# Kernel tuning notes

Measured on AMD Instinct MI355X. Metric: run time of the kernel, lower is better.

Reference implementation:

```python
import jax, jax.numpy as jnp
import numpy as np

B, L, HID = 2, 2048, 4096
NH, NKV, HD = 16, 4, 64
BLOCK = 16
THETA = 8000000.0
EPS = 1e-6
NEG = jnp.finfo(jnp.float32).min


def _rope_tables(theta, L, hd):
    inv_freq = 1.0 / (theta ** (np.arange(0, hd, 2, dtype=np.float32) / hd))  # [hd/2]
    t = np.arange(L, dtype=np.float32)
    freqs = np.outer(t, inv_freq)                      # [L, hd/2]
    emb = np.concatenate([freqs, freqs], axis=-1)      # [L, hd]
    return jnp.asarray(np.cos(emb)), jnp.asarray(np.sin(emb))


def setup_inputs() -> dict:
    key = jax.random.key(0)
    k1, k2, k3 = jax.random.split(key, 3)
    hidden_states = jax.random.normal(k1, (B, L, HID), dtype=jnp.float32)
    Wqkv = jax.random.normal(k2, (HID, (NH + 2 * NKV) * HD), dtype=jnp.float32) * 0.006
    Wo = jax.random.normal(k3, (NH * HD, HID), dtype=jnp.float32) * 0.006
    q_norm_w = jnp.ones((HD,), dtype=jnp.float32)
    k_norm_w = jnp.ones((HD,), dtype=jnp.float32)
    # block-diagonal causal additive mask [1,1,L,L]
    idx = jnp.arange(L)
    same_block = (idx[:, None] // BLOCK) == (idx[None, :] // BLOCK)
    causal = idx[:, None] >= idx[None, :]
    attention_mask = jnp.where(same_block & causal, 0.0, NEG)[None, None].astype(jnp.float32)
    cos1, sin1 = _rope_tables(THETA, L, HD)
    cos = jnp.broadcast_to(cos1[None], (B, L, HD))
    sin = jnp.broadcast_to(sin1[None], (B, L, HD))
    return {"hidden_states": hidden_states, "attention_mask": attention_mask,
            "cos": cos, "sin": sin, "Wqkv": Wqkv, "Wo": Wo,
            "q_norm_w": q_norm_w, "k_norm_w": k_norm_w}


def _rms_norm(x, w):
    xf = x.astype(jnp.float32)
    var = jnp.mean(xf * xf, axis=-1, keepdims=True)
    return (xf * jax.lax.rsqrt(var + EPS)).astype(x.dtype) * w


def _rotate_half(x):
    x1, x2 = jnp.split(x, 2, axis=-1)
    return jnp.concatenate([-x2, x1], axis=-1)


def reference(hidden_states, attention_mask, cos, sin, Wqkv, Wo, q_norm_w, k_norm_w):
    Bc, Lc, _ = hidden_states.shape
    qkv = hidden_states @ Wqkv                                # [B,L,(NH+2NKV)*HD]
    qkv = qkv.reshape(Bc, Lc, NH + 2 * NKV, HD)
    q, k, v = jnp.split(qkv, [NH, NH + NKV], axis=2)
    q = q.transpose(0, 2, 1, 3)                               # [B,NH,L,HD]
    k = k.transpose(0, 2, 1, 3)                               # [B,NKV,L,HD]
    v = v.transpose(0, 2, 1, 3)
    q = _rms_norm(q, q_norm_w)
    k = _rms_norm(k, k_norm_w)
    c = cos[:, None]                                          # [B,1,L,HD]
    s = sin[:, None]
    q = q * c + _rotate_half(q) * s
    k = k * c + _rotate_half(k) * s
    groups = NH // NKV
    k = jnp.repeat(k, groups, axis=1)                         # [B,NH,L,HD]
    v = jnp.repeat(v, groups, axis=1)
    scale = 1.0 / jnp.sqrt(jnp.float32(HD))
    scores = jnp.einsum('bhqd,bhkd->bhqk', q, k) * scale + attention_mask
    probs = jax.nn.softmax(scores, axis=-1)
    out = jnp.einsum('bhqk,bhkd->bhqd', probs, v)             # [B,NH,L,HD]
    out = out.transpose(0, 2, 1, 3).reshape(Bc, Lc, NH * HD)
    return out @ Wo
```

## Files before the change

### kernel.cpp

```cpp
#include <hip/hip_runtime.h>
#include <hip/hip_bf16.h>
#include <cstdint>

#define B_SZ   2
#define L_SEQ  2048
#define HID    4096
#define NH     16
#define NKV    4
#define HD     64
#define NQKV   (NH + 2*NKV)
#define QKV_N  (NQKV*HD)
#define O_N    (NH*HD)
#define M_ROWS (B_SZ*L_SEQ)
#define EPSV   1e-6f

typedef __bf16  bf16x8_t  __attribute__((ext_vector_type(8)));
typedef float   f32x4_t   __attribute__((ext_vector_type(4)));
typedef unsigned short ushort8_t __attribute__((ext_vector_type(8)));

__device__ __forceinline__ unsigned short f2b(float f) {
    union { float f; uint32_t u; } v; v.f = f;
    uint32_t r = v.u + 0x7FFFu + ((v.u >> 16) & 1u);
    return (unsigned short)(r >> 16);
}
__device__ __forceinline__ float b2f(unsigned short u) {
    union { uint32_t u; float f; } v; v.u = ((uint32_t)u) << 16;
    return v.f;
}

__device__ __forceinline__ void gload_lds16(const void* g, void* l) {
    __builtin_amdgcn_global_load_lds(
        (__attribute__((address_space(1))) void*)(g),
        (__attribute__((address_space(3))) void*)(l),
        16, 0, 0);
}

#define BARF() do { asm volatile("" ::: "memory"); \
                    __builtin_amdgcn_s_barrier();  \
                    asm volatile("" ::: "memory"); } while (0)

template <int N> __device__ __forceinline__ void vmcnt_wait() {
    if constexpr (N == 4)       asm volatile("s_waitcnt vmcnt(4)"  ::: "memory");
    else if constexpr (N == 5)  asm volatile("s_waitcnt vmcnt(5)"  ::: "memory");
    else if constexpr (N == 6)  asm volatile("s_waitcnt vmcnt(6)"  ::: "memory");
    else if constexpr (N == 8)  asm volatile("s_waitcnt vmcnt(8)"  ::: "memory");
    else if constexpr (N == 12) asm volatile("s_waitcnt vmcnt(12)" ::: "memory");
    else                        asm volatile("s_waitcnt vmcnt(0)"  ::: "memory");
}

__global__ __launch_bounds__(256) void cvt_f32_bf16(const float* __restrict__ in,
                                                    unsigned short* __restrict__ out,
                                                    int n8) {
    int i = blockIdx.x * 256 + threadIdx.x;
    if (i >= n8) return;
    const float4* p = (const float4*)(in + (size_t)i * 8);
    float4 a = p[0], b = p[1];
    ushort8_t o;
    o[0]=f2b(a.x); o[1]=f2b(a.y); o[2]=f2b(a.z); o[3]=f2b(a.w);
    o[4]=f2b(b.x); o[5]=f2b(b.y); o[6]=f2b(b.z); o[7]=f2b(b.w);
    *(ushort8_t*)(out + (size_t)i * 8) = o;
}

__global__ __launch_bounds__(256) void transpose_both(const float* __restrict__ Wqkv,
                                                      unsigned short* __restrict__ WqkvT,
                                                      const float* __restrict__ Wo,
                                                      unsigned short* __restrict__ WoT) {
    __shared__ float t[32][33];
    const float* in;
    unsigned short* out;
    int R, C, bx, by;
    if (blockIdx.x < 6144) {
        in = Wqkv; out = WqkvT; R = HID; C = QKV_N;
        bx = blockIdx.x % 48; by = blockIdx.x / 48;
    } else {
        int b = blockIdx.x - 6144;
        in = Wo; out = WoT; R = O_N; C = HID;
        bx = b % 128; by = b / 128;
    }
    const int c0 = bx * 32;
    const int r0 = by * 32;
    const int tx = threadIdx.x & 31;
    const int ty = threadIdx.x >> 5;
    #pragma unroll
    for (int i = 0; i < 32; i += 8)
        t[ty + i][tx] = in[(size_t)(r0 + ty + i) * C + c0 + tx];
    __syncthreads();
    #pragma unroll
    for (int i = 0; i < 32; i += 8)
        out[(size_t)(c0 + ty + i) * R + r0 + tx] = f2b(t[tx][ty + i]);
}

template <int BM, int BN, int BK, int NBUF, int NWM, int NWN, bool OBF16, typename OutT>
__global__ __launch_bounds__(512, 2)
void gemm_sb(const unsigned short* __restrict__ A,
             const unsigned short* __restrict__ Bt,
             OutT* __restrict__ C, int M, int N, int K) {
    constexpr int WM    = BM / NWM;
    constexpr int WN    = BN / NWN;
    constexpr int AF    = WM / 16;
    constexpr int BF    = WN / 16;
    constexpr int KK    = BK / 32;
    constexpr int BUF   = (BM + BN) * BK;
    constexpr int ROWS  = 4096 / BK;
    constexpr int AR    = BM / ROWS;
    constexpr int BR    = BN / ROWS;
    constexpr int RNDS  = AR + BR;
    constexpr int DEPTH = NBUF - 2;

    __shared__ unsigned short smem[NBUF * BUF];

    const int tid  = threadIdx.x;
    const int lane = tid & 63;
    const int wave = tid >> 6;
    const int wm   = wave / NWN;
    const int wn   = wave % NWN;
    const int fr   = lane & 15;
    const int fq   = lane >> 4;

    const int nbx = N / BN;
    int bid = blockIdx.x;
    const int cpx = gridDim.x >> 3;
    bid = (bid & 7) * cpx + (bid >> 3);
    const int bx = bid % nbx, by = bid / nbx;
    const int m0 = by * BM, n0 = bx * BN;

    const int srow = tid / (BK / 8);
    const int sch  = tid & (BK / 8 - 1);
    const int ssw  = (BK == 64) ? (srow & 7) : ((srow >> 1) & 3);
    const int scs  = (sch ^ ssw) << 3;
    const unsigned short* gA = A  + (size_t)(m0 + srow) * K + scs;
    const unsigned short* gB = Bt + (size_t)(n0 + srow) * K + scs;

    const int frsw = (BK == 64) ? (fr & 7) : ((fr >> 1) & 3);

    f32x4_t acc[AF][BF];
    #pragma unroll
    for (int m = 0; m < AF; m++)
        #pragma unroll
        for (int n = 0; n < BF; n++)
            acc[m][n] = (f32x4_t){0.f, 0.f, 0.f, 0.f};

    const int NT = K / BK;

    auto STAGE = [&](int T) {
        const int pb = (T % NBUF) * BUF;
        #pragma unroll
        for (int q = 0; q < AR; ++q)
            gload_lds16(gA + (size_t)(q * ROWS) * K + (size_t)T * BK,
                        &smem[pb + q * 4096 + tid * 8]);
        #pragma unroll
        for (int q = 0; q < BR; ++q)
            gload_lds16(gB + (size_t)(q * ROWS) * K + (size_t)T * BK,
                        &smem[pb + BM * BK + q * 4096 + tid * 8]);
    };

    #pragma unroll
    for (int pt = 0; pt < NBUF - 1; ++pt) STAGE(pt);
    vmcnt_wait<DEPTH * RNDS>();

    for (int t = 0; t < NT; ++t) {
        const int sb = (t % NBUF) * BUF;
        BARF();

        #pragma unroll
        for (int kk = 0; kk < KK; ++kk) {
            const int cxk = (((kk * 4 + fq) ^ frsw)) << 3;
            bf16x8_t aF[AF], bF[BF];
            #pragma unroll
            for (int mm = 0; mm < AF; ++mm)
                aF[mm] = *(const bf16x8_t*)&smem[sb + (wm*WM + mm*16 + fr)*BK + cxk];
            #pragma unroll
            for (int nn = 0; nn < BF; ++nn)
                bF[nn] = *(const bf16x8_t*)&smem[sb + BM*BK + (wn*WN + nn*16 + fr)*BK + cxk];

            if (kk == 0 && t + NBUF - 1 < NT) STAGE(t + NBUF - 1);

            __builtin_amdgcn_s_setprio(1);
            #pragma unroll
            for (int mm = 0; mm < AF; ++mm)
                #pragma unroll
                for (int nn = 0; nn < BF; ++nn)
                    acc[mm][nn] = __builtin_amdgcn_mfma_f32_16x16x32_bf16(
                        aF[mm], bF[nn], acc[mm][nn], 0, 0, 0);
            __builtin_amdgcn_s_setprio(0);
        }

        if constexpr (DEPTH == 2) {
            if (t + 3 < NT)      { vmcnt_wait<2 * RNDS>(); }
            else if (t + 2 < NT) { vmcnt_wait<RNDS>(); }
            else if (t + 1 < NT) { vmcnt_wait<0>(); }
        } else {
            if (t + 2 < NT)      { vmcnt_wait<RNDS>(); }
            else if (t + 1 < NT) { vmcnt_wait<0>(); }
        }
    }

    const int crow = m0 + wm * WM + fq * 4;
    const int ccol = n0 + wn * WN + fr;
    #pragma unroll
    for (int m = 0; m < AF; m++)
        #pragma unroll
        for (int n = 0; n < BF; n++)
            #pragma unroll
            for (int rr = 0; rr < 4; rr++) {
                const size_t idx = (size_t)(crow + m*16 + rr) * N + ccol + n*16;
                if constexpr (OBF16) C[idx] = (OutT)f2b(acc[m][n][rr]);
                else                 C[idx] = (OutT)acc[m][n][rr];
            }
}

__global__ __launch_bounds__(64) void attn_fused(const unsigned short* __restrict__ qkv,
                                                 const float* __restrict__ cosb,
                                                 const float* __restrict__ sinb,
                                                 const float* __restrict__ qw,
                                                 const float* __restrict__ kw,
                                                 unsigned short* __restrict__ out) {
    const int h    = blockIdx.x & (NH - 1);
    const int blk  = (blockIdx.x >> 4) & 127;
    const int b    = blockIdx.x >> 11;
    const int pos0 = blk * 16;
    const int kvh  = h >> 2;

    const int lane = threadIdx.x;
    const int r    = lane >> 2;
    const int qp   = lane & 3;
    const int d0   = qp * 16;

    __shared__ float qs[16][65];
    __shared__ float ks[16][65];
    __shared__ float vs[16][65];
    __shared__ float ps[16][17];

    const size_t rowb = ((size_t)(b * L_SEQ + pos0 + r)) * NQKV;
    const unsigned short* qptr = qkv + (rowb + h) * HD + d0;
    const unsigned short* kptr = qkv + (rowb + NH + kvh) * HD + d0;
    const unsigned short* vptr = qkv + (rowb + NH + NKV + kvh) * HD + d0;
    const size_t csrow = ((size_t)(b * L_SEQ + pos0 + r)) * HD + d0;

    float q[16], k[16], v[16], cs[16], sn[16];
    {
        ushort8_t q0 = *(const ushort8_t*)&qptr[0], q1 = *(const ushort8_t*)&qptr[8];
        ushort8_t k0 = *(const ushort8_t*)&kptr[0], k1 = *(const ushort8_t*)&kptr[8];
        ushort8_t v0 = *(const ushort8_t*)&vptr[0], v1 = *(const ushort8_t*)&vptr[8];
        #pragma unroll
        for (int i = 0; i < 8; i++) {
            q[i] = b2f(q0[i]); q[i+8] = b2f(q1[i]);
            k[i] = b2f(k0[i]); k[i+8] = b2f(k1[i]);
            v[i] = b2f(v0[i]); v[i+8] = b2f(v1[i]);
        }
        #pragma unroll
        for (int i = 0; i < 16; i += 4) {
            *(float4*)&cs[i] = *(const float4*)&cosb[csrow + i];
            *(float4*)&sn[i] = *(const float4*)&sinb[csrow + i];
        }
    }

    float sq = 0.f, sk = 0.f;
    #pragma unroll
    for (int i = 0; i < 16; i++) { sq += q[i]*q[i]; sk += k[i]*k[i]; }
    sq += __shfl_xor(sq, 1); sq += __shfl_xor(sq, 2);
    sk += __shfl_xor(sk, 1); sk += __shfl_xor(sk, 2);
    const float rq = rsqrtf(sq * (1.f / HD) + EPSV);
    const float rk = rsqrtf(sk * (1.f / HD) + EPSV);

    const float sgn = (qp < 2) ? -1.f : 1.f;
    #pragma unroll
    for (int i = 0; i < 16; i++) {
        float qn = q[i] * rq * qw[d0 + i];
        float kn = k[i] * rk * kw[d0 + i];
        float qo = __shfl_xor(qn, 2);
        float ko = __shfl_xor(kn, 2);
        qs[r][d0 + i] = qn * cs[i] + sgn * qo * sn[i];
        ks[r][d0 + i] = kn * cs[i] + sgn * ko * sn[i];
        vs[r][d0 + i] = v[i];
    }
    __syncthreads();

    float sc[4] = {0.f, 0.f, 0.f, 0.f};
    for (int d = 0; d < 64; d++) {
        const float qd = qs[r][d];
        sc[0] += qd * ks[qp     ][d];
        sc[1] += qd * ks[qp +  4][d];
        sc[2] += qd * ks[qp +  8][d];
        sc[3] += qd * ks[qp + 12][d];
    }
    #pragma unroll
    for (int cc = 0; cc < 4; cc++) {
        const int c = qp + cc * 4;
        sc[cc] = (c <= r) ? sc[cc] * 0.125f : -3.0e38f;
    }
    float mx = fmaxf(fmaxf(sc[0], sc[1]), fmaxf(sc[2], sc[3]));
    mx = fmaxf(mx, __shfl_xor(mx, 1));
    mx = fmaxf(mx, __shfl_xor(mx, 2));
    float e[4], sum = 0.f;
    #pragma unroll
    for (int cc = 0; cc < 4; cc++) { e[cc] = __expf(sc[cc] - mx); sum += e[cc]; }
    sum += __shfl_xor(sum, 1); sum += __shfl_xor(sum, 2);
    const float inv = 1.f / sum;
    #pragma unroll
    for (int cc = 0; cc < 4; cc++) ps[r][qp + cc * 4] = e[cc] * inv;
    __syncthreads();

    float o[16];
    #pragma unroll
    for (int i = 0; i < 16; i++) o[i] = 0.f;
    #pragma unroll
    for (int c = 0; c < 16; c++) {
        const float p = ps[r][c];
        #pragma unroll
        for (int i = 0; i < 16; i++) o[i] += p * vs[c][d0 + i];
    }

    __attribute__((aligned(16))) unsigned short ob[16];
    #pragma unroll
    for (int i = 0; i < 16; i++) ob[i] = f2b(o[i]);
    unsigned short* optr = out + (((size_t)(b * L_SEQ + pos0 + r) * NH + h) * HD) + d0;
    *(uint4*)optr       = *(uint4*)&ob[0];
    *((uint4*)optr + 1) = *(uint4*)&ob[8];
}

extern "C" void kernel_launch(void* const* d_in, const int* in_sizes, int n_in,
                              void* d_out, int out_size, void* d_ws, size_t ws_size,
                              hipStream_t stream) {
    const float* hid  = (const float*)d_in[0];
    const float* cosb = (const float*)d_in[2];
    const float* sinb = (const float*)d_in[3];
    const float* Wqkv = (const float*)d_in[4];
    const float* Wo   = (const float*)d_in[5];
    const float* qw   = (const float*)d_in[6];
    const float* kw   = (const float*)d_in[7];
    float* outp = (float*)d_out;

    char* ws = (char*)d_ws;
    unsigned short* Hb    = (unsigned short*)ws; ws += (size_t)M_ROWS * HID * 2;
    unsigned short* WqkvT = (unsigned short*)ws; ws += (size_t)QKV_N * HID * 2;
    unsigned short* WoT   = (unsigned short*)ws; ws += (size_t)HID * O_N * 2;
    unsigned short* qkvb  = (unsigned short*)ws; ws += (size_t)M_ROWS * QKV_N * 2;
    unsigned short* attnb = (unsigned short*)ws;

    {
        int n8 = (M_ROWS * HID) / 8;
        cvt_f32_bf16<<<(n8 + 255) / 256, 256, 0, stream>>>(hid, Hb, n8);
    }
    transpose_both<<<dim3(6144 + 4096), 256, 0, stream>>>(Wqkv, WqkvT, Wo, WoT);

    gemm_sb<128, 192, 64, 3, 2, 4, true, unsigned short>
        <<<dim3((M_ROWS / 128) * (QKV_N / 192)), 512, 0, stream>>>
        (Hb, WqkvT, qkvb, M_ROWS, QKV_N, HID);

    attn_fused<<<dim3(B_SZ * (L_SEQ / 16) * NH), 64, 0, stream>>>(qkvb, cosb, sinb, qw, kw, attnb);

    gemm_sb<256, 256, 32, 4, 2, 4, false, float>
        <<<dim3((M_ROWS / 256) * (HID / 256)), 512, 0, stream>>>
        (attnb, WoT, outp, M_ROWS, HID, O_N);
}
```

Baseline: 145.8 us.

## Replace output-projection GEMM with 8-phase ping-pong pipelined kernel

Swaps the generic gemm_sb used for the Wo projection for a specialized 256x256 tile kernel with a BK=64 double-buffered LDS, XOR-swizzled layout, and an 8-phase schedule that interleaves direct global-to-LDS loads with MFMA groups, using s_setprio around the math. It also remaps block IDs across 8 groups for L2 locality. The goal is better overlap of memory and compute in the second GEMM, at the cost of many barriers and 64KB of LDS per block, which may limit occupancy.

```diff
diff --git a/kernel.cpp b/kernel.cpp
--- a/kernel.cpp
+++ b/kernel.cpp
@@ -38,6 +38,7 @@
 #define BARF() do { asm volatile("" ::: "memory"); \
                     __builtin_amdgcn_s_barrier();  \
                     asm volatile("" ::: "memory"); } while (0)
+#define LGKMW() asm volatile("s_waitcnt lgkmcnt(0)" ::: "memory")
 
 template <int N> __device__ __forceinline__ void vmcnt_wait() {
     if constexpr (N == 4)       asm volatile("s_waitcnt vmcnt(4)"  ::: "memory");
@@ -209,6 +210,120 @@
             }
 }
 
+#define G2_BUF 32768
+
+__global__ __launch_bounds__(512, 2)
+void gemm2_8p(const unsigned short* __restrict__ A,
+              const unsigned short* __restrict__ Bt,
+              float* __restrict__ C) {
+    constexpr int K     = O_N;
+    constexpr int N     = HID;
+    constexpr int NT    = K / 64;
+    constexpr int NITER = NT / 2;
+
+    __shared__ unsigned short smem[2 * G2_BUF];
+
+    const int tid  = threadIdx.x;
+    const int lane = tid & 63;
+    const int wave = tid >> 6;
+    const int wm   = wave >> 2;
+    const int wn   = wave & 3;
+    const int fr   = lane & 15;
+    const int fq   = lane >> 4;
+
+    const int nbx = N >> 8;
+    int bid = blockIdx.x;
+    const int cpx = gridDim.x >> 3;
+    bid = (bid & 7) * cpx + (bid >> 3);
+    const int bx = bid % nbx, by = bid / nbx;
+    const int m0 = by << 8, n0 = bx << 8;
+
+    const int srow = tid >> 3;
+    const int scs  = ((tid & 7) ^ (srow & 7)) << 3;
+    const unsigned short* gA = A  + (size_t)(m0 + srow) * K + scs;
+    const unsigned short* gB = Bt + (size_t)(n0 + srow) * K + scs;
+    const int frsw = fr & 7;
+
+    f32x4_t acc[8][4];
+    #pragma unroll
+    for (int m = 0; m < 8; m++)
+        #pragma unroll
+        for (int n = 0; n < 4; n++)
+            acc[m][n] = (f32x4_t){0.f, 0.f, 0.f, 0.f};
+
+#define SA(T, q) gload_lds16(gA + (size_t)((q)*64)*K + (size_t)(T)*64, \
+                             &smem[((T)&1)*G2_BUF + (q)*4096 + tid*8])
+#define SB(T, q) gload_lds16(gB + (size_t)((q)*64)*K + (size_t)(T)*64, \
+                             &smem[((T)&1)*G2_BUF + 16384 + (q)*4096 + tid*8])
+#define RDA(T, MH, KI) { _Pragma("unroll") for (int mm = 0; mm < 4; ++mm) { \
+    const int ro = ((T)&1)*G2_BUF + (wm*128 + (MH)*64 + mm*16 + fr)*64; \
+    aF[mm] = *(const bf16x8_t*)&smem[ro + ((((KI)*4 + fq) ^ frsw) << 3)]; } }
+#define RDB(T, KI, dst) { _Pragma("unroll") for (int nn = 0; nn < 4; ++nn) { \
+    const int ro = ((T)&1)*G2_BUF + 16384 + (wn*64 + nn*16 + fr)*64; \
+    dst[nn] = *(const bf16x8_t*)&smem[ro + ((((KI)*4 + fq) ^ frsw) << 3)]; } }
+#define MM16(MH, BS) { __builtin_amdgcn_s_setprio(1); \
+    _Pragma("unroll") for (int mm = 0; mm < 4; ++mm) \
+    _Pragma("unroll") for (int nn = 0; nn < 4; ++nn) \
+        acc[(MH)*4 + mm][nn] = __builtin_amdgcn_mfma_f32_16x16x32_bf16( \
+            aF[mm], BS[nn], acc[(MH)*4 + mm][nn], 0, 0, 0); \
+    __builtin_amdgcn_s_setprio(0); }
+
+    SA(0,0); SA(0,1); SA(0,2); SA(0,3);
+    SB(0,0); SB(0,1); SB(0,2); SB(0,3);
+    SA(1,0); SA(1,2); SB(1,0); SB(1,1);
+    vmcnt_wait<4>();
+    BARF();
+
+    for (int i = 0; i < NITER; ++i) {
+        const int t0 = 2*i, t1 = 2*i + 1;
+        bf16x8_t aF[4], b0[4], b1[4];
+
+        RDA(t0, 0, 0); RDB(t0, 0, b0);
+        SA(t1, 1); SA(t1, 3);
+        BARF(); LGKMW(); MM16(0, b0); BARF();
+        RDA(t0, 0, 1); RDB(t0, 1, b1);
+        SB(t1, 2); SB(t1, 3);
+        BARF(); LGKMW(); MM16(0, b1); BARF();
+        RDA(t0, 1, 0);
+        if (t0 + 2 < NT) { SA(t0 + 2, 0); SA(t0 + 2, 2); }
+        BARF(); LGKMW(); MM16(1, b0); BARF();
+        RDA(t0, 1, 1);
+        if (t0 + 2 < NT) { SB(t0 + 2, 0); SB(t0 + 2, 1); }
+        BARF(); LGKMW(); MM16(1, b1);
+        if (i + 1 < NITER) { vmcnt_wait<4>(); } else { vmcnt_wait<0>(); }
+        BARF();
+        RDA(t1, 0, 0); RDB(t1, 0, b0);
+        if (t0 + 2 < NT) { SA(t0 + 2, 1); SA(t0 + 2, 3); }
+        BARF(); LGKMW(); MM16(0, b0); BARF();
+        RDA(t1, 0, 1); RDB(t1, 1, b1);
+        if (t0 + 2 < NT) { SB(t0 + 2, 2); SB(t0 + 2, 3); }
+        BARF(); LGKMW(); MM16(0, b1); BARF();
+        RDA(t1, 1, 0);
+        if (t1 + 2 < NT) { SA(t1 + 2, 0); SA(t1 + 2, 2); }
+        BARF(); LGKMW(); MM16(1, b0); BARF();
+        RDA(t1, 1, 1);
+        if (t1 + 2 < NT) { SB(t1 + 2, 0); SB(t1 + 2, 1); }
+        BARF(); LGKMW(); MM16(1, b1);
+        if (i + 1 < NITER) { vmcnt_wait<4>(); }
+        BARF();
+    }
+#undef SA
+#undef SB
+#undef RDA
+#undef RDB
+#undef MM16
+
+    const int crow = m0 + wm * 128 + fq * 4;
+    const int ccol = n0 + wn * 64 + fr;
+    #pragma unroll
+    for (int m = 0; m < 8; m++)
+        #pragma unroll
+        for (int n = 0; n < 4; n++)
+            #pragma unroll
+            for (int rr = 0; rr < 4; rr++)
+                C[(size_t)(crow + m*16 + rr) * N + ccol + n*16] = acc[m][n][rr];
+}
+
 __global__ __launch_bounds__(64) void attn_fused(const unsigned short* __restrict__ qkv,
                                                  const float* __restrict__ cosb,
                                                  const float* __restrict__ sinb,
@@ -350,7 +465,6 @@
 
     attn_fused<<<dim3(B_SZ * (L_SEQ / 16) * NH), 64, 0, stream>>>(qkvb, cosb, sinb, qw, kw, attnb);
 
-    gemm_sb<256, 256, 32, 4, 2, 4, false, float>
-        <<<dim3((M_ROWS / 256) * (HID / 256)), 512, 0, stream>>>
-        (attnb, WoT, outp, M_ROWS, HID, O_N);
-}
+    gemm2_8p<<<dim3((M_ROWS / 256) * (HID / 256)), 512, 0, stream>>>
+        (attnb, WoT, outp);
+}
```

New measurement: 144.5 us. About the same (-0.9%).

## Add dedicated 128x128 output-projection GEMM and merge prep kernels into one launch

Applied to the files above, without the earlier changes.

Replaces the generic 256x256-tile output projection GEMM with a specialized 128x128-tile kernel. It uses 256 threads, double-buffered direct-to-LDS loads, an XOR-swizzled LDS layout and an LDS-staged coalesced float4 epilogue, giving four times more blocks for better CU occupancy and load balance. It also fuses the hidden-state conversion and weight transpose into a single prep launch to cut launch overhead. The smaller tile lowers data reuse per block, and the two-stage pipeline with full vmcnt waits may expose memory latency.

```diff
diff --git a/kernel.cpp b/kernel.cpp
--- a/kernel.cpp
+++ b/kernel.cpp
@@ -38,6 +38,7 @@
 #define BARF() do { asm volatile("" ::: "memory"); \
                     __builtin_amdgcn_s_barrier();  \
                     asm volatile("" ::: "memory"); } while (0)
+#define LGKMW() asm volatile("s_waitcnt lgkmcnt(0)" ::: "memory")
 
 template <int N> __device__ __forceinline__ void vmcnt_wait() {
     if constexpr (N == 4)       asm volatile("s_waitcnt vmcnt(4)"  ::: "memory");
@@ -48,34 +49,35 @@
     else                        asm volatile("s_waitcnt vmcnt(0)"  ::: "memory");
 }
 
-__global__ __launch_bounds__(256) void cvt_f32_bf16(const float* __restrict__ in,
-                                                    unsigned short* __restrict__ out,
-                                                    int n8) {
-    int i = blockIdx.x * 256 + threadIdx.x;
-    if (i >= n8) return;
-    const float4* p = (const float4*)(in + (size_t)i * 8);
-    float4 a = p[0], b = p[1];
-    ushort8_t o;
-    o[0]=f2b(a.x); o[1]=f2b(a.y); o[2]=f2b(a.z); o[3]=f2b(a.w);
-    o[4]=f2b(b.x); o[5]=f2b(b.y); o[6]=f2b(b.z); o[7]=f2b(b.w);
-    *(ushort8_t*)(out + (size_t)i * 8) = o;
-}
-
-__global__ __launch_bounds__(256) void transpose_both(const float* __restrict__ Wqkv,
-                                                      unsigned short* __restrict__ WqkvT,
-                                                      const float* __restrict__ Wo,
-                                                      unsigned short* __restrict__ WoT) {
+#define CVT_BLKS 8192
+__global__ __launch_bounds__(256) void prep(const float* __restrict__ hid,
+                                            unsigned short* __restrict__ Hb,
+                                            const float* __restrict__ Wqkv,
+                                            unsigned short* __restrict__ WqkvT,
+                                            const float* __restrict__ Wo,
+                                            unsigned short* __restrict__ WoT) {
+    if (blockIdx.x < CVT_BLKS) {
+        int i = blockIdx.x * 256 + threadIdx.x;
+        const float4* p = (const float4*)(hid + (size_t)i * 8);
+        float4 a = p[0], b = p[1];
+        ushort8_t o;
+        o[0]=f2b(a.x); o[1]=f2b(a.y); o[2]=f2b(a.z); o[3]=f2b(a.w);
+        o[4]=f2b(b.x); o[5]=f2b(b.y); o[6]=f2b(b.z); o[7]=f2b(b.w);
+        *(ushort8_t*)(Hb + (size_t)i * 8) = o;
+        return;
+    }
     __shared__ float t[32][33];
     const float* in;
     unsigned short* out;
     int R, C, bx, by;
-    if (blockIdx.x < 6144) {
+    int blk = blockIdx.x - CVT_BLKS;
+    if (blk < 6144) {
         in = Wqkv; out = WqkvT; R = HID; C = QKV_N;
-        bx = blockIdx.x % 48; by = blockIdx.x / 48;
+        bx = blk % 48; by = blk / 48;
     } else {
-        int b = blockIdx.x - 6144;
+        blk -= 6144;
         in = Wo; out = WoT; R = O_N; C = HID;
-        bx = b % 128; by = b / 128;
+        bx = blk % 128; by = blk / 128;
     }
     const int c0 = bx * 32;
     const int r0 = by * 32;
@@ -209,6 +211,115 @@
             }
 }
 
+__global__ __launch_bounds__(256, 2)
+void gemm2_tlp(const unsigned short* __restrict__ A,
+               const unsigned short* __restrict__ Bt,
+               float* __restrict__ C) {
+    constexpr int K   = O_N;
+    constexpr int N   = HID;
+    constexpr int NT  = K / 64;
+    constexpr int BUF = 16384;
+
+    __shared__ unsigned short smem[2 * BUF];
+
+    const int tid  = threadIdx.x;
+    const int lane = tid & 63;
+    const int wave = tid >> 6;
+    const int wm   = wave >> 1;
+    const int wn   = wave & 1;
+    const int fr   = lane & 15;
+    const int fq   = lane >> 4;
+
+    const int nbx = N >> 7;
+    int bid = blockIdx.x;
+    const int cpx = gridDim.x >> 3;
+    bid = (bid & 7) * cpx + (bid >> 3);
+    const int bx = bid % nbx, by = bid / nbx;
+    const int m0 = by << 7, n0 = bx << 7;
+
+    const int srow = tid >> 3;
+    const int scs  = ((tid & 7) ^ (srow & 7)) << 3;
+    const unsigned short* gA = A  + (size_t)(m0 + srow) * K + scs;
+    const unsigned short* gB = Bt + (size_t)(n0 + srow) * K + scs;
+    const int frsw = fr & 7;
+
+    f32x4_t acc[4][4];
+    #pragma unroll
+    for (int m = 0; m < 4; m++)
+        #pragma unroll
+        for (int n = 0; n < 4; n++)
+            acc[m][n] = (f32x4_t){0.f, 0.f, 0.f, 0.f};
+
+    auto STAGE = [&](int T) {
+        const int pb = (T & 1) * BUF;
+        #pragma unroll
+        for (int q = 0; q < 4; ++q)
+            gload_lds16(gA + (size_t)(q * 32) * K + (size_t)T * 64,
+                        &smem[pb + q * 2048 + tid * 8]);
+        #pragma unroll
+        for (int q = 0; q < 4; ++q)
+            gload_lds16(gB + (size_t)(q * 32) * K + (size_t)T * 64,
+                        &smem[pb + 8192 + q * 2048 + tid * 8]);
+    };
+
+    STAGE(0);
+    vmcnt_wait<0>();
+
+    for (int t = 0; t < NT; ++t) {
+        const int sb = (t & 1) * BUF;
+        BARF();
+
+        #pragma unroll
+        for (int kk = 0; kk < 2; ++kk) {
+            const int cxk = (((kk * 4 + fq) ^ frsw)) << 3;
+            bf16x8_t aF[4], bF[4];
+            #pragma unroll
+            for (int mm = 0; mm < 4; ++mm)
+                aF[mm] = *(const bf16x8_t*)&smem[sb + (wm*64 + mm*16 + fr)*64 + cxk];
+            #pragma unroll
+            for (int nn = 0; nn < 4; ++nn)
+                bF[nn] = *(const bf16x8_t*)&smem[sb + 8192 + (wn*64 + nn*16 + fr)*64 + cxk];
+
+            if (kk == 0 && t + 1 < NT) STAGE(t + 1);
+
+            __builtin_amdgcn_s_setprio(1);
+            #pragma unroll
+            for (int mm = 0; mm < 4; ++mm)
+                #pragma unroll
+                for (int nn = 0; nn < 4; ++nn)
+                    acc[mm][nn] = __builtin_amdgcn_mfma_f32_16x16x32_bf16(
+                        aF[mm], bF[nn], acc[mm][nn], 0, 0, 0);
+            __builtin_amdgcn_s_setprio(0);
+        }
+
+        if (t + 1 < NT) vmcnt_wait<0>();
+    }
+
+    float* lf = (float*)smem;
+    BARF();
+    #pragma unroll
+    for (int m = 0; m < 4; m++)
+        #pragma unroll
+        for (int n = 0; n < 4; n++)
+            #pragma unroll
+            for (int rr = 0; rr < 4; rr++) {
+                const int row = wm*64 + m*16 + fq*4 + rr;
+                const int col = wn*64 + n*16 + fr;
+                lf[row*128 + (col ^ ((row & 7) << 2))] = acc[m][n][rr];
+            }
+    BARF();
+    #pragma unroll
+    for (int s = 0; s < 8; s++) {
+        const int row = s*16 + (tid >> 4);
+        const int sw  = (row & 7) << 2;
+        const int c0  = (tid & 15) * 4;
+        const float4 v0 = *(const float4*)&lf[row*128 + ((c0     ) ^ sw)];
+        const float4 v1 = *(const float4*)&lf[row*128 + ((c0 + 64) ^ sw)];
+        *(float4*)&C[(size_t)(m0 + row) * N + n0 + c0]      = v0;
+        *(float4*)&C[(size_t)(m0 + row) * N + n0 + c0 + 64] = v1;
+    }
+}
+
 __global__ __launch_bounds__(64) void attn_fused(const unsigned short* __restrict__ qkv,
                                                  const float* __restrict__ cosb,
                                                  const float* __restrict__ sinb,
@@ -338,11 +449,8 @@
     unsigned short* qkvb  = (unsigned short*)ws; ws += (size_t)M_ROWS * QKV_N * 2;
     unsigned short* attnb = (unsigned short*)ws;
 
-    {
-        int n8 = (M_ROWS * HID) / 8;
-        cvt_f32_bf16<<<(n8 + 255) / 256, 256, 0, stream>>>(hid, Hb, n8);
-    }
-    transpose_both<<<dim3(6144 + 4096), 256, 0, stream>>>(Wqkv, WqkvT, Wo, WoT);
+    prep<<<dim3(CVT_BLKS + 6144 + 4096), 256, 0, stream>>>
+        (hid, Hb, Wqkv, WqkvT, Wo, WoT);
 
     gemm_sb<128, 192, 64, 3, 2, 4, true, unsigned short>
         <<<dim3((M_ROWS / 128) * (QKV_N / 192)), 512, 0, stream>>>
@@ -350,7 +458,6 @@
 
     attn_fused<<<dim3(B_SZ * (L_SEQ / 16) * NH), 64, 0, stream>>>(qkvb, cosb, sinb, qw, kw, attnb);
 
-    gemm_sb<256, 256, 32, 4, 2, 4, false, float>
-        <<<dim3((M_ROWS / 256) * (HID / 256)), 512, 0, stream>>>
-        (attnb, WoT, outp, M_ROWS, HID, O_N);
-}
+    gemm2_tlp<<<dim3((M_ROWS / 128) * (HID / 128)), 256, 0, stream>>>
+        (attnb, WoT, outp);
+}
```

Measured after the change: 147.4 us. Within noise of the previous version (+1.1%).
